# Kernel tuning notes

Measured on AMD Instinct MI355X. Metric: run time of the kernel, lower is better.

The kernel has to match this reference:

```python
import jax, jax.numpy as jnp
import numpy as np

B = 2048        # number of independent sample paths (batched simulation)
DIM = 64        # SDE state dimension
NSTEPS = 500    # Euler steps: (t1-t0)/dt0 = 1.0/0.002
DT0 = 0.002


def setup_inputs() -> dict:
    key = jax.random.key(0)
    ks = jax.random.split(key, 6)
    s = 0.5 / np.sqrt(DIM)  # keep the linear SDE stable over the horizon
    return {
        "x0": jax.random.normal(ks[0], (B, DIM), jnp.float32),
        # raw N(0,1) noise; scaled by sqrt(dt) inside reference (Brownian increments)
        "dW": jax.random.normal(ks[1], (B, NSTEPS, DIM), jnp.float32),
        "drift": jax.random.normal(ks[2], (DIM, DIM), jnp.float32) * s,
        "drift_bias": jax.random.normal(ks[3], (DIM,), jnp.float32) * 0.1,
        "diffusion": jax.random.normal(ks[4], (DIM, DIM), jnp.float32) * (0.1 * s),
        "diffusion_bias": jax.random.normal(ks[5], (DIM,), jnp.float32) * 0.1,
        "ts": jnp.arange(NSTEPS + 1, dtype=jnp.float32) * DT0,
    }


def reference(x0, dW, drift, drift_bias, diffusion, diffusion_bias, ts):
    """Euler-Maruyama for dx = (A x + b) dt + diag(C x + d) dW.

    Matches the diffrax Euler solver with SaveAt(ts) where ts lies on the
    fixed-step grid. diag(C x + d) @ dW == (C x + d) * dW elementwise.
    Returns ys: [B, NSTEPS+1, DIM] (saved states at every ts, incl. x0).
    """
    dts = jnp.diff(ts)                       # [NSTEPS]
    dW_t = jnp.swapaxes(dW, 0, 1)            # [NSTEPS, B, DIM]

    def step(x, inp):
        dt, dw = inp
        drift_v = x @ drift.T + drift_bias                 # [B, DIM]
        diff_v = x @ diffusion.T + diffusion_bias          # [B, DIM]
        x_next = x + dt * drift_v + diff_v * (jnp.sqrt(dt) * dw)
        return x_next, x_next

    _, ys = jax.lax.scan(step, x0, (dts, dW_t))            # [NSTEPS, B, DIM]
    ys = jnp.concatenate([x0[None], ys], axis=0)           # [NSTEPS+1, B, DIM]
    return jnp.swapaxes(ys, 0, 1)                          # [B, NSTEPS+1, DIM]
```

## Files before the change

kernel.cpp:

```cpp
#include <hip/hip_runtime.h>

#define NPATH  2048
#define DIM    64
#define NSTEPS 500
#define PPW    16

typedef __attribute__((ext_vector_type(8))) short bf16x8;
typedef __attribute__((ext_vector_type(4))) float f32x4;

union FragU { bf16x8 v; unsigned int u[4]; uint4 q; };

__device__ __forceinline__ unsigned int pk_bf16(float lo, float hi) {
    unsigned int r;
    asm("v_cvt_pk_bf16_f32 %0, %1, %2" : "=v"(r) : "v"(lo), "v"(hi));
    return r;
}

__attribute__((amdgpu_waves_per_eu(1, 4)))
__global__ __launch_bounds__(256) void sde_mfma_mw_kernel(
    const float* __restrict__ x0,
    const float* __restrict__ dW,
    const float* __restrict__ drift,
    const float* __restrict__ drift_bias,
    const float* __restrict__ diffusion,
    const float* __restrict__ diffusion_bias,
    const float* __restrict__ ts,
    float* __restrict__ out)
{
    __shared__ __align__(16) unsigned short xt[2][PPW * DIM];
    __shared__ float2 dtp[NSTEPS];

    const int tid   = threadIdx.x;
    const int wn    = tid >> 6;
    const int lane  = tid & 63;
    const int c     = lane & 15;
    const int h     = lane >> 4;
    const int pbase = blockIdx.x * PPW;
    const int mydim = 16 * wn + c;

    for (int i = tid; i < NSTEPS; i += 256) {
        const float d = ts[i + 1] - ts[i];
        dtp[i] = make_float2(d, sqrtf(d));
    }

    FragU bd0, bd1, bs0, bs1;
    {
        const float* Ar = drift     + mydim * DIM + 8 * h;
        const float* Cr = diffusion + mydim * DIM + 8 * h;
        float4 t;
        t = *(const float4*)(Ar +  0); bd0.u[0] = pk_bf16(t.x, t.y); bd0.u[1] = pk_bf16(t.z, t.w);
        t = *(const float4*)(Ar +  4); bd0.u[2] = pk_bf16(t.x, t.y); bd0.u[3] = pk_bf16(t.z, t.w);
        t = *(const float4*)(Ar + 32); bd1.u[0] = pk_bf16(t.x, t.y); bd1.u[1] = pk_bf16(t.z, t.w);
        t = *(const float4*)(Ar + 36); bd1.u[2] = pk_bf16(t.x, t.y); bd1.u[3] = pk_bf16(t.z, t.w);
        t = *(const float4*)(Cr +  0); bs0.u[0] = pk_bf16(t.x, t.y); bs0.u[1] = pk_bf16(t.z, t.w);
        t = *(const float4*)(Cr +  4); bs0.u[2] = pk_bf16(t.x, t.y); bs0.u[3] = pk_bf16(t.z, t.w);
        t = *(const float4*)(Cr + 32); bs1.u[0] = pk_bf16(t.x, t.y); bs1.u[1] = pk_bf16(t.z, t.w);
        t = *(const float4*)(Cr + 36); bs1.u[2] = pk_bf16(t.x, t.y); bs1.u[3] = pk_bf16(t.z, t.w);
    }
    const float bdr = drift_bias[mydim];
    const float bdi = diffusion_bias[mydim];

    float xst[4];
    const float* dwq[4];
    float* op[4];
    unsigned int woff[4];
#pragma unroll
    for (int j = 0; j < 4; ++j) {
        const int pp = 4 * h + j;
        const int p  = pbase + pp;
        dwq[j] = dW  + (size_t)p * NSTEPS * DIM + mydim;
        op[j]  = out + (size_t)p * (NSTEPS + 1) * DIM + mydim;
        woff[j] = (unsigned)((pp * 32 + ((mydim >> 1) ^ ((pp & 7) << 2))) * 2 + (c & 1));
        const float v = x0[p * DIM + mydim];
        xst[j] = v;
        __builtin_nontemporal_store(v, op[j]);
        xt[0][woff[j]] = (unsigned short)pk_bf16(v, v);
    }

    const int ra0 = c * 8 + (h ^ (c & 7));
    const int ra1 = c * 8 + ((4 + h) ^ (c & 7));
    const uint4* xr0 = (const uint4*)xt[0];
    const uint4* xr1 = (const uint4*)xt[1];
    unsigned short* xw0 = xt[0];
    unsigned short* xw1 = xt[1];

    float R0[4], R1[4], R2[4], R3[4];
#pragma unroll
    for (int j = 0; j < 4; ++j) {
        R0[j] = dwq[j][0 * DIM];
        R1[j] = dwq[j][1 * DIM];
        R2[j] = dwq[j][2 * DIM];
        R3[j] = dwq[j][3 * DIM];
        dwq[j] += 4 * DIM;
    }

    __syncthreads();

#define STEP(S, R, PF, XR, XW, KOFF)                                          \
    {                                                                         \
        const float2 dtc = dtp[S];                                            \
        FragU a0, a1;                                                         \
        a0.q = XR[ra0];                                                       \
        a1.q = XR[ra1];                                                       \
        f32x4 adr = {bdr, bdr, bdr, bdr};                                     \
        f32x4 adi = {bdi, bdi, bdi, bdi};                                     \
        adr = __builtin_amdgcn_mfma_f32_16x16x32_bf16(a0.v, bd0.v, adr, 0, 0, 0); \
        adr = __builtin_amdgcn_mfma_f32_16x16x32_bf16(a1.v, bd1.v, adr, 0, 0, 0); \
        adi = __builtin_amdgcn_mfma_f32_16x16x32_bf16(a0.v, bs0.v, adi, 0, 0, 0); \
        adi = __builtin_amdgcn_mfma_f32_16x16x32_bf16(a1.v, bs1.v, adi, 0, 0, 0); \
        _Pragma("unroll")                                                     \
        for (int j = 0; j < 4; ++j) {                                         \
            const float xn = fmaf(dtc.x, adr[j], xst[j])                      \
                             + adi[j] * (dtc.y * R[j]);                       \
            xst[j] = xn;                                                      \
            __builtin_nontemporal_store(xn, op[j] + (size_t)((S) + 1) * DIM); \
            XW[woff[j]] = (unsigned short)pk_bf16(xn, xn);                    \
        }                                                                     \
        if (PF) {                                                             \
            _Pragma("unroll")                                                 \
            for (int j = 0; j < 4; ++j) R[j] = dwq[j][(KOFF) * DIM];          \
        }                                                                     \
        asm volatile("s_waitcnt lgkmcnt(0)" ::: "memory");                    \
        __builtin_amdgcn_s_barrier();                                         \
        __builtin_amdgcn_sched_barrier(0);                                    \
    }

    for (int it = 0; it < NSTEPS / 4 - 1; ++it) {
        const int s = it * 4;
        STEP(s + 0, R0, 1, xr0, xw1, 0)
        STEP(s + 1, R1, 1, xr1, xw0, 1)
        STEP(s + 2, R2, 1, xr0, xw1, 2)
        STEP(s + 3, R3, 1, xr1, xw0, 3)
#pragma unroll
        for (int j = 0; j < 4; ++j) dwq[j] += 4 * DIM;
    }
    {
        const int s = NSTEPS - 4;
        STEP(s + 0, R0, 0, xr0, xw1, 0)
        STEP(s + 1, R1, 0, xr1, xw0, 1)
        STEP(s + 2, R2, 0, xr0, xw1, 2)
        STEP(s + 3, R3, 0, xr1, xw0, 3)
    }
#undef STEP
}

extern "C" void kernel_launch(void* const* d_in, const int* in_sizes, int n_in,
                              void* d_out, int out_size, void* d_ws, size_t ws_size,
                              hipStream_t stream) {
    const float* x0             = (const float*)d_in[0];
    const float* dW             = (const float*)d_in[1];
    const float* drift          = (const float*)d_in[2];
    const float* drift_bias     = (const float*)d_in[3];
    const float* diffusion      = (const float*)d_in[4];
    const float* diffusion_bias = (const float*)d_in[5];
    const float* ts             = (const float*)d_in[6];
    float* out = (float*)d_out;

    dim3 grid(NPATH / PPW);
    dim3 block(256);
    hipLaunchKernelGGL(sde_mfma_mw_kernel, grid, block, 0, stream,
                       x0, dW, drift, drift_bias, diffusion, diffusion_bias,
                       ts, out);
}
```

Baseline: 151.0 us.

## Break MFMA accumulation chain, deepen dW prefetch to eight steps

Each K-half matmul now runs as an independent MFMA with its own accumulator (bias or zero), and the two halves are summed afterwards. This removes the back-to-back MFMA dependency on the serial per-step critical path. The dW prefetch ring grows from four to eight steps, and each step issues its prefetch before the MFMAs. The next dt/sqrt(dt) pair is loaded one step ahead, and output pointers are incremented instead of recomputed. The cost is more VGPRs and a couple of extra adds per element, and the launch bounds change to a single block per CU hint.

```diff
diff --git a/kernel.cpp b/kernel.cpp
--- a/kernel.cpp
+++ b/kernel.cpp
@@ -16,8 +16,9 @@
     return r;
 }
 
-__attribute__((amdgpu_waves_per_eu(1, 4)))
-__global__ __launch_bounds__(256) void sde_mfma_mw_kernel(
+#define MFMA __builtin_amdgcn_mfma_f32_16x16x32_bf16
+
+__global__ __launch_bounds__(256, 1) void sde_mfma_mw2_kernel(
     const float* __restrict__ x0,
     const float* __restrict__ dW,
     const float* __restrict__ drift,
@@ -28,7 +29,7 @@
     float* __restrict__ out)
 {
     __shared__ __align__(16) unsigned short xt[2][PPW * DIM];
-    __shared__ float2 dtp[NSTEPS];
+    __shared__ float2 dtp[NSTEPS + 1];
 
     const int tid   = threadIdx.x;
     const int wn    = tid >> 6;
@@ -42,6 +43,7 @@
         const float d = ts[i + 1] - ts[i];
         dtp[i] = make_float2(d, sqrtf(d));
     }
+    if (tid == 0) dtp[NSTEPS] = make_float2(0.f, 0.f);
 
     FragU bd0, bd1, bs0, bs1;
     {
@@ -59,6 +61,9 @@
     }
     const float bdr = drift_bias[mydim];
     const float bdi = diffusion_bias[mydim];
+    const f32x4 cbA = {bdr, bdr, bdr, bdr};
+    const f32x4 cbC = {bdi, bdi, bdi, bdi};
+    const f32x4 cz  = {0.f, 0.f, 0.f, 0.f};
 
     float xst[4];
     const float* dwq[4];
@@ -74,6 +79,7 @@
         const float v = x0[p * DIM + mydim];
         xst[j] = v;
         __builtin_nontemporal_store(v, op[j]);
+        op[j] += DIM;
         xt[0][woff[j]] = (unsigned short)pk_bf16(v, v);
     }
 
@@ -84,62 +90,85 @@
     unsigned short* xw0 = xt[0];
     unsigned short* xw1 = xt[1];
 
-    float R0[4], R1[4], R2[4], R3[4];
+    float R0[4], R1[4], R2[4], R3[4], R4[4], R5[4], R6[4], R7[4];
 #pragma unroll
     for (int j = 0; j < 4; ++j) {
-        R0[j] = dwq[j][0 * DIM];
-        R1[j] = dwq[j][1 * DIM];
-        R2[j] = dwq[j][2 * DIM];
-        R3[j] = dwq[j][3 * DIM];
-        dwq[j] += 4 * DIM;
+        R0[j] = dwq[j][0 * DIM]; R1[j] = dwq[j][1 * DIM];
+        R2[j] = dwq[j][2 * DIM]; R3[j] = dwq[j][3 * DIM];
+        R4[j] = dwq[j][4 * DIM]; R5[j] = dwq[j][5 * DIM];
+        R6[j] = dwq[j][6 * DIM]; R7[j] = dwq[j][7 * DIM];
+        dwq[j] += 8 * DIM;
     }
 
     __syncthreads();
 
-#define STEP(S, R, PF, XR, XW, KOFF)                                          \
+    float2 dts = dtp[0];
+
+#define STEP(S, R, PF, KOFF, XR, XW)                                          \
     {                                                                         \
-        const float2 dtc = dtp[S];                                            \
         FragU a0, a1;                                                         \
         a0.q = XR[ra0];                                                       \
         a1.q = XR[ra1];                                                       \
-        f32x4 adr = {bdr, bdr, bdr, bdr};                                     \
-        f32x4 adi = {bdi, bdi, bdi, bdi};                                     \
-        adr = __builtin_amdgcn_mfma_f32_16x16x32_bf16(a0.v, bd0.v, adr, 0, 0, 0); \
-        adr = __builtin_amdgcn_mfma_f32_16x16x32_bf16(a1.v, bd1.v, adr, 0, 0, 0); \
-        adi = __builtin_amdgcn_mfma_f32_16x16x32_bf16(a0.v, bs0.v, adi, 0, 0, 0); \
-        adi = __builtin_amdgcn_mfma_f32_16x16x32_bf16(a1.v, bs1.v, adi, 0, 0, 0); \
+        const float srw0 = dts.y * R[0];   \
+        const float srw1 = dts.y * R[1];                                      \
+        const float srw2 = dts.y * R[2];                                      \
+        const float srw3 = dts.y * R[3];                                      \
+        if (PF) {                                                             \
+            R[0] = dwq[0][(KOFF) * DIM];                                      \
+            R[1] = dwq[1][(KOFF) * DIM];                                      \
+            R[2] = dwq[2][(KOFF) * DIM];                                      \
+            R[3] = dwq[3][(KOFF) * DIM];                                      \
+        }                                                                     \
+        const float2 dtn = dtp[(S) + 1];                                      \
+        const f32x4 adA = MFMA(a0.v, bd0.v, cbA, 0, 0, 0);                    \
+        const f32x4 adB = MFMA(a1.v, bd1.v, cz,  0, 0, 0);                    \
+        const f32x4 ciA = MFMA(a0.v, bs0.v, cbC, 0, 0, 0);                    \
+        const f32x4 ciB = MFMA(a1.v, bs1.v, cz,  0, 0, 0);                    \
+        const float srw[4] = {srw0, srw1, srw2, srw3};                        \
         _Pragma("unroll")                                                     \
         for (int j = 0; j < 4; ++j) {                                         \
-            const float xn = fmaf(dtc.x, adr[j], xst[j])                      \
-                             + adi[j] * (dtc.y * R[j]);                       \
+            const float ad = adA[j] + adB[j];                                 \
+            const float ci = ciA[j] + ciB[j];                                 \
+            const float xn = fmaf(dts.x, ad, xst[j]) + ci * srw[j];           \
             xst[j] = xn;                                                      \
-            __builtin_nontemporal_store(xn, op[j] + (size_t)((S) + 1) * DIM); \
+            __builtin_nontemporal_store(xn, op[j]);                           \
+            op[j] += DIM;                                                     \
             XW[woff[j]] = (unsigned short)pk_bf16(xn, xn);                    \
         }                                                                     \
-        if (PF) {                                                             \
-            _Pragma("unroll")                                                 \
-            for (int j = 0; j < 4; ++j) R[j] = dwq[j][(KOFF) * DIM];          \
-        }                                                                     \
+        dts = dtn;                                                            \
         asm volatile("s_waitcnt lgkmcnt(0)" ::: "memory");                    \
         __builtin_amdgcn_s_barrier();                                         \
         __builtin_amdgcn_sched_barrier(0);                                    \
     }
 
-    for (int it = 0; it < NSTEPS / 4 - 1; ++it) {
-        const int s = it * 4;
-        STEP(s + 0, R0, 1, xr0, xw1, 0)
-        STEP(s + 1, R1, 1, xr1, xw0, 1)
-        STEP(s + 2, R2, 1, xr0, xw1, 2)
-        STEP(s + 3, R3, 1, xr1, xw0, 3)
+    for (int it = 0; it < 61; ++it) {
+        const int s = it * 8;
+        STEP(s + 0, R0, 1, 0, xr0, xw1)
+        STEP(s + 1, R1, 1, 1, xr1, xw0)
+        STEP(s + 2, R2, 1, 2, xr0, xw1)
+        STEP(s + 3, R3, 1, 3, xr1, xw0)
+        STEP(s + 4, R4, 1, 4, xr0, xw1)
+        STEP(s + 5, R5, 1, 5, xr1, xw0)
+        STEP(s + 6, R6, 1, 6, xr0, xw1)
+        STEP(s + 7, R7, 1, 7, xr1, xw0)
 #pragma unroll
-        for (int j = 0; j < 4; ++j) dwq[j] += 4 * DIM;
+        for (int j = 0; j < 4; ++j) dwq[j] += 8 * DIM;
     }
     {
-        const int s = NSTEPS - 4;
-        STEP(s + 0, R0, 0, xr0, xw1, 0)
-        STEP(s + 1, R1, 0, xr1, xw0, 1)
-        STEP(s + 2, R2, 0, xr0, xw1, 2)
-        STEP(s + 3, R3, 0, xr1, xw0, 3)
+        STEP(488, R0, 1, 0, xr0, xw1)
+        STEP(489, R1, 1, 1, xr1, xw0)
+        STEP(490, R2, 1, 2, xr0, xw1)
+        STEP(491, R3, 1, 3, xr1, xw0)
+        STEP(492, R4, 0, 0, xr0, xw1)
+        STEP(493, R5, 0, 0, xr1, xw0)
+        STEP(494, R6, 0, 0, xr0, xw1)
+        STEP(495, R7, 0, 0, xr1, xw0)
+    }
+    {
+        STEP(496, R0, 0, 0, xr0, xw1)
+        STEP(497, R1, 0, 0, xr1, xw0)
+        STEP(498, R2, 0, 0, xr0, xw1)
+        STEP(499, R3, 0, 0, xr1, xw0)
     }
 #undef STEP
 }
@@ -158,7 +187,7 @@
 
     dim3 grid(NPATH / PPW);
     dim3 block(256);
-    hipLaunchKernelGGL(sde_mfma_mw_kernel, grid, block, 0, stream,
+    hipLaunchKernelGGL(sde_mfma_mw2_kernel, grid, block, 0, stream,
                        x0, dW, drift, drift_bias, diffusion, diffusion_bias,
                        ts, out);
 }
```

Result: faster. 138.2 us, median of 2 (-8.5%).
